# Kernel tuning notes

Hardware: AMD Instinct MI355X
Metric: run time of the kernel (lower is better)

The kernel has to match this reference:

```python
import jax, jax.numpy as jnp
import numpy as np

TF_ALPHA = 0.125  # teacher-forcing blend used in forward()


def setup_inputs() -> dict:
    key = jax.random.key(0)
    ks = jax.random.split(key, 6)
    B, T, dx, dz, dy = 512, 1024, 32, 64, 256
    return {
        "X": jax.random.normal(ks[0], (B, T, dx), dtype=jnp.float32),
        "A": (jax.random.normal(ks[1], (dz,), dtype=jnp.float32) * 0.1),
        "W1": jax.random.normal(ks[2], (dz, dy), dtype=jnp.float32) / np.sqrt(dy).astype(np.float32),
        "W2": jax.random.normal(ks[3], (dy, dz), dtype=jnp.float32) / np.sqrt(dz).astype(np.float32),
        "h1": jax.random.normal(ks[4], (dz,), dtype=jnp.float32) * 0.01,
        "h2": jax.random.normal(ks[5], (dy,), dtype=jnp.float32) * 0.01,
    }


def reference(X, A, W1, W2, h1, h2):
    # X: (batch, time, dim_x); shallow-PLRNN, dim_x_proj=0, no mean centering, no inputs.
    B, T, dx = X.shape
    dz = A.shape[0]

    def teacher_force(z, f, alpha):
        # blend forcing signal into first dx latent dims where f is not NaN
        blend = alpha * f + (1.0 - alpha) * z[:, :dx]
        return z.at[:, :dx].set(jnp.where(jnp.isnan(f), z[:, :dx], blend))

    # z0 = teacher_force(zeros, X[:,0], alpha=1)
    z0 = teacher_force(jnp.zeros((B, dz), X.dtype), X[:, 0], 1.0)

    Xt = jnp.transpose(X, (1, 0, 2))  # (T, B, dx)

    def step(z, x_t):
        zf = teacher_force(z, x_t, TF_ALPHA)
        # shallow-PLRNN: z' = A*z + W1 @ relu(W2 @ z + h2) + h1
        hidden = jax.nn.relu(jnp.einsum('yz,bz->by', W2, zf) + h2)
        z_new = A * zf + jnp.einsum('zy,by->bz', W1, hidden) + h1
        return z_new, z_new

    _, Z = jax.lax.scan(step, z0, Xt)          # (T, B, dz)
    Z = jnp.transpose(Z, (1, 0, 2))            # (B, T, dz)
    return Z[:, :, :dx]                        # output = first dim_x latent dims
```

## Files before the change

kernel.cpp:

```cpp
#include <hip/hip_runtime.h>

#define BB 512
#define TT 1024
#define DX 32
#define DZ 64
#define DY 256
#define ALPHA 0.125f

template<int CTRL>
__device__ __forceinline__ float qperm_add(float x) {
    int p = __builtin_amdgcn_update_dpp(0, __float_as_int(x), CTRL, 0xF, 0xF, true);
    return x + __int_as_float(p);
}
__device__ __forceinline__ float quad_allreduce(float x) {
    x = qperm_add<0xB1>(x);
    x = qperm_add<0x4E>(x);
    return x;
}

__global__ __launch_bounds__(256, 2)
void plrnn_scan(const float* __restrict__ X, const float* __restrict__ A,
                const float* __restrict__ W1, const float* __restrict__ W2,
                const float* __restrict__ h1, const float* __restrict__ h2,
                float* __restrict__ out) {
    const int b   = blockIdx.x;
    const int tid = threadIdx.x;

    const int j  = tid >> 2;
    const int s  = tid & 3;
    const int p  = (tid >> 2) & 15;
    const int c  = tid & 3;
    const int wv = tid >> 6;
    const int s2 = (wv << 2) | c;

    __shared__ float zf_s[DZ];
    __shared__ float hid_s[DY];
    __shared__ float part_s[4 * 68];

    float4 w2c[16];
    float4 w1c[16];
#pragma unroll
    for (int k = 0; k < 16; ++k) {
        w2c[k] = make_float4(W2[(4 * j + 0) * DZ + 16 * s + k],
                             W2[(4 * j + 1) * DZ + 16 * s + k],
                             W2[(4 * j + 2) * DZ + 16 * s + k],
                             W2[(4 * j + 3) * DZ + 16 * s + k]);
        w1c[k] = make_float4(W1[(4 * p + 0) * DY + 16 * s2 + k],
                             W1[(4 * p + 1) * DY + 16 * s2 + k],
                             W1[(4 * p + 2) * DY + 16 * s2 + k],
                             W1[(4 * p + 3) * DY + 16 * s2 + k]);
    }
    const float4 h2q = make_float4(h2[4 * j + 0], h2[4 * j + 1],
                                   h2[4 * j + 2], h2[4 * j + 3]);
    const float Ar  = (tid < DZ) ? A[tid]  : 0.0f;
    const float h1r = (tid < DZ) ? h1[tid] : 0.0f;

    const float* Xb = X   + (size_t)b * TT * DX;
    float*       Ob = out + (size_t)b * TT * DX;

    float zfreg = 0.0f;
    if (tid < DZ) {
        float zf = 0.0f;
        if (tid < DX) { float x0 = Xb[tid]; zf = (x0 == x0) ? x0 : 0.0f; }
        zfreg = zf;
        zf_s[tid] = zf;
    }
    __syncthreads();

    for (int t = 0; t < TT; ++t) {
        float xnext = 0.0f;
        if (tid < DX && (t + 1) < TT) xnext = Xb[(t + 1) * DX + tid];

        float zl[16];
        {
            const float4* zp = (const float4*)zf_s + 4 * s;
            *(float4*)&zl[0]  = zp[0];
            *(float4*)&zl[4]  = zp[1];
            *(float4*)&zl[8]  = zp[2];
            *(float4*)&zl[12] = zp[3];
        }
        float ax = 0.f, ay = 0.f, az = 0.f, aw = 0.f;
#pragma unroll
        for (int k = 0; k < 16; ++k) {
            ax = fmaf(w2c[k].x, zl[k], ax);
            ay = fmaf(w2c[k].y, zl[k], ay);
            az = fmaf(w2c[k].z, zl[k], az);
            aw = fmaf(w2c[k].w, zl[k], aw);
        }
        ax = quad_allreduce(ax);
        ay = quad_allreduce(ay);
        az = quad_allreduce(az);
        aw = quad_allreduce(aw);
        if (s == 0) {
            float4 hv = make_float4(fmaxf(ax + h2q.x, 0.f), fmaxf(ay + h2q.y, 0.f),
                                    fmaxf(az + h2q.z, 0.f), fmaxf(aw + h2q.w, 0.f));
            *(float4*)&hid_s[4 * j] = hv;
        }
        __syncthreads();

        float hl[16];
        {
            const float4* hp = (const float4*)hid_s + 4 * s2;
            *(float4*)&hl[0]  = hp[0];
            *(float4*)&hl[4]  = hp[1];
            *(float4*)&hl[8]  = hp[2];
            *(float4*)&hl[12] = hp[3];
        }
        float px = 0.f, py = 0.f, pz = 0.f, pw = 0.f;
#pragma unroll
        for (int k = 0; k < 16; ++k) {
            px = fmaf(w1c[k].x, hl[k], px);
            py = fmaf(w1c[k].y, hl[k], py);
            pz = fmaf(w1c[k].z, hl[k], pz);
            pw = fmaf(w1c[k].w, hl[k], pw);
        }
        px = quad_allreduce(px);
        py = quad_allreduce(py);
        pz = quad_allreduce(pz);
        pw = quad_allreduce(pw);
        if (c == 0) {
            *(float4*)&part_s[wv * 68 + 4 * p] = make_float4(px, py, pz, pw);
        }
        __syncthreads();

        if (tid < DZ) {
            float ssum = (part_s[tid] + part_s[68 + tid]) +
                         (part_s[136 + tid] + part_s[204 + tid]);
            float znew = fmaf(Ar, zfreg, ssum + h1r);
            float zf = znew;
            if (tid < DX) {
                Ob[t * DX + tid] = znew;
                zf = (xnext == xnext) ? fmaf(ALPHA, xnext, (1.0f - ALPHA) * znew)
                                      : znew;
            }
            zfreg = zf;
            zf_s[tid] = zf;
        }
        __syncthreads();
    }
}

extern "C" void kernel_launch(void* const* d_in, const int* in_sizes, int n_in,
                              void* d_out, int out_size, void* d_ws, size_t ws_size,
                              hipStream_t stream) {
    const float* X  = (const float*)d_in[0];
    const float* A  = (const float*)d_in[1];
    const float* W1 = (const float*)d_in[2];
    const float* W2 = (const float*)d_in[3];
    const float* h1 = (const float*)d_in[4];
    const float* h2 = (const float*)d_in[5];
    float* out = (float*)d_out;

    plrnn_scan<<<BB, 256, 0, stream>>>(X, A, W1, W2, h1, h2, out);
}
```

Before: 888.5 us.

## Repartition PLRNN step across 512 threads and drop the partial-sum barrier

Doubles the block to 512 threads so each thread holds half as many weights and runs a 32-FMA dot product per matvec instead of 64. Each hidden unit is computed by a lane pair, and each latent output by a group of 8 lanes reduced entirely with DPP ops. This removes the shared-memory partial-sum stage and one of the three barriers per time step. The hidden buffer is padded per wave to avoid LDS bank conflicts. In exchange there are more waves per CU and more threads taking part in each barrier.

```diff
diff --git a/kernel.cpp b/kernel.cpp
--- a/kernel.cpp
+++ b/kernel.cpp
@@ -6,19 +6,15 @@
 #define DZ 64
 #define DY 256
 #define ALPHA 0.125f
+#define HP 36
 
 template<int CTRL>
-__device__ __forceinline__ float qperm_add(float x) {
+__device__ __forceinline__ float dpp_add(float x) {
     int p = __builtin_amdgcn_update_dpp(0, __float_as_int(x), CTRL, 0xF, 0xF, true);
     return x + __int_as_float(p);
 }
-__device__ __forceinline__ float quad_allreduce(float x) {
-    x = qperm_add<0xB1>(x);
-    x = qperm_add<0x4E>(x);
-    return x;
-}
 
-__global__ __launch_bounds__(256, 2)
+__global__ __launch_bounds__(512, 4)
 void plrnn_scan(const float* __restrict__ X, const float* __restrict__ A,
                 const float* __restrict__ W1, const float* __restrict__ W2,
                 const float* __restrict__ h1, const float* __restrict__ h2,
@@ -26,115 +22,85 @@
     const int b   = blockIdx.x;
     const int tid = threadIdx.x;
 
-    const int j  = tid >> 2;
-    const int s  = tid & 3;
-    const int p  = (tid >> 2) & 15;
-    const int c  = tid & 3;
-    const int wv = tid >> 6;
-    const int s2 = (wv << 2) | c;
+    const int y    = tid >> 1;
+    const int half = tid & 1;
+    const int z    = tid >> 3;
+    const int oct  = tid & 7;
+    const int wv   = tid >> 6;
 
     __shared__ float zf_s[DZ];
-    __shared__ float hid_s[DY];
-    __shared__ float part_s[4 * 68];
+    __shared__ float hid_s[8 * HP];
 
-    float4 w2c[16];
-    float4 w1c[16];
+    float4 w2r[8];
+    float4 w1r[8];
 #pragma unroll
-    for (int k = 0; k < 16; ++k) {
-        w2c[k] = make_float4(W2[(4 * j + 0) * DZ + 16 * s + k],
-                             W2[(4 * j + 1) * DZ + 16 * s + k],
-                             W2[(4 * j + 2) * DZ + 16 * s + k],
-                             W2[(4 * j + 3) * DZ + 16 * s + k]);
-        w1c[k] = make_float4(W1[(4 * p + 0) * DY + 16 * s2 + k],
-                             W1[(4 * p + 1) * DY + 16 * s2 + k],
-                             W1[(4 * p + 2) * DY + 16 * s2 + k],
-                             W1[(4 * p + 3) * DY + 16 * s2 + k]);
+    for (int j = 0; j < 8; ++j) {
+        w2r[j] = *(const float4*)&W2[y * DZ + 32 * half + 4 * j];
+        w1r[j] = *(const float4*)&W1[z * DY + 32 * oct + 4 * j];
     }
-    const float4 h2q = make_float4(h2[4 * j + 0], h2[4 * j + 1],
-                                   h2[4 * j + 2], h2[4 * j + 3]);
-    const float Ar  = (tid < DZ) ? A[tid]  : 0.0f;
-    const float h1r = (tid < DZ) ? h1[tid] : 0.0f;
+    const float h2r = h2[y];
+    const float Ar  = A[z];
+    const float h1r = h1[z];
 
     const float* Xb = X   + (size_t)b * TT * DX;
     float*       Ob = out + (size_t)b * TT * DX;
 
     float zfreg = 0.0f;
-    if (tid < DZ) {
+    if (oct == 0) {
         float zf = 0.0f;
-        if (tid < DX) { float x0 = Xb[tid]; zf = (x0 == x0) ? x0 : 0.0f; }
+        if (z < DX) { float x0 = Xb[z]; zf = (x0 == x0) ? x0 : 0.0f; }
         zfreg = zf;
-        zf_s[tid] = zf;
+        zf_s[z] = zf;
     }
     __syncthreads();
 
+    const int hidx = wv * HP + (y & 31);
+    const float* w2f = (const float*)w2r;
+    const float* w1f = (const float*)w1r;
+
     for (int t = 0; t < TT; ++t) {
         float xnext = 0.0f;
-        if (tid < DX && (t + 1) < TT) xnext = Xb[(t + 1) * DX + tid];
+        if (oct == 0 && z < DX && (t + 1) < TT) xnext = Xb[(t + 1) * DX + z];
 
-        float zl[16];
-        {
-            const float4* zp = (const float4*)zf_s + 4 * s;
-            *(float4*)&zl[0]  = zp[0];
-            *(float4*)&zl[4]  = zp[1];
-            *(float4*)&zl[8]  = zp[2];
-            *(float4*)&zl[12] = zp[3];
+        const float4* zp = (const float4*)(zf_s + 32 * half);
+        float a0 = 0.f, a1 = 0.f, a2 = 0.f, a3 = 0.f;
+#pragma unroll
+        for (int j = 0; j < 8; ++j) {
+            float4 v = zp[j];
+            a0 = fmaf(w2f[4 * j + 0], v.x, a0);
+            a1 = fmaf(w2f[4 * j + 1], v.y, a1);
+            a2 = fmaf(w2f[4 * j + 2], v.z, a2);
+            a3 = fmaf(w2f[4 * j + 3], v.w, a3);
         }
-        float ax = 0.f, ay = 0.f, az = 0.f, aw = 0.f;
-#pragma unroll
-        for (int k = 0; k < 16; ++k) {
-            ax = fmaf(w2c[k].x, zl[k], ax);
-            ay = fmaf(w2c[k].y, zl[k], ay);
-            az = fmaf(w2c[k].z, zl[k], az);
-            aw = fmaf(w2c[k].w, zl[k], aw);
-        }
-        ax = quad_allreduce(ax);
-        ay = quad_allreduce(ay);
-        az = quad_allreduce(az);
-        aw = quad_allreduce(aw);
-        if (s == 0) {
-            float4 hv = make_float4(fmaxf(ax + h2q.x, 0.f), fmaxf(ay + h2q.y, 0.f),
-                                    fmaxf(az + h2q.z, 0.f), fmaxf(aw + h2q.w, 0.f));
-            *(float4*)&hid_s[4 * j] = hv;
-        }
+        float d1 = (a0 + a1) + (a2 + a3);
+        d1 = dpp_add<0xB1>(d1);
+        if (half == 0) hid_s[hidx] = fmaxf(d1 + h2r, 0.0f);
         __syncthreads();
 
-        float hl[16];
-        {
-            const float4* hp = (const float4*)hid_s + 4 * s2;
-            *(float4*)&hl[0]  = hp[0];
-            *(float4*)&hl[4]  = hp[1];
-            *(float4*)&hl[8]  = hp[2];
-            *(float4*)&hl[12] = hp[3];
+        const float4* hp = (const float4*)(hid_s + HP * oct);
+        float p0 = 0.f, p1 = 0.f, p2 = 0.f, p3 = 0.f;
+#pragma unroll
+        for (int j = 0; j < 8; ++j) {
+            float4 v = hp[j];
+            p0 = fmaf(w1f[4 * j + 0], v.x, p0);
+            p1 = fmaf(w1f[4 * j + 1], v.y, p1);
+            p2 = fmaf(w1f[4 * j + 2], v.z, p2);
+            p3 = fmaf(w1f[4 * j + 3], v.w, p3);
         }
-        float px = 0.f, py = 0.f, pz = 0.f, pw = 0.f;
-#pragma unroll
-        for (int k = 0; k < 16; ++k) {
-            px = fmaf(w1c[k].x, hl[k], px);
-            py = fmaf(w1c[k].y, hl[k], py);
-            pz = fmaf(w1c[k].z, hl[k], pz);
-            pw = fmaf(w1c[k].w, hl[k], pw);
-        }
-        px = quad_allreduce(px);
-        py = quad_allreduce(py);
-        pz = quad_allreduce(pz);
-        pw = quad_allreduce(pw);
-        if (c == 0) {
-            *(float4*)&part_s[wv * 68 + 4 * p] = make_float4(px, py, pz, pw);
-        }
-        __syncthreads();
-
-        if (tid < DZ) {
-            float ssum = (part_s[tid] + part_s[68 + tid]) +
-                         (part_s[136 + tid] + part_s[204 + tid]);
-            float znew = fmaf(Ar, zfreg, ssum + h1r);
+        float d2 = (p0 + p1) + (p2 + p3);
+        d2 = dpp_add<0xB1>(d2);
+        d2 = dpp_add<0x4E>(d2);
+        d2 = dpp_add<0x141>(d2);
+        if (oct == 0) {
+            float znew = fmaf(Ar, zfreg, d2 + h1r);
             float zf = znew;
-            if (tid < DX) {
-                Ob[t * DX + tid] = znew;
+            if (z < DX) {
+                Ob[t * DX + z] = znew;
                 zf = (xnext == xnext) ? fmaf(ALPHA, xnext, (1.0f - ALPHA) * znew)
                                       : znew;
             }
             zfreg = zf;
-            zf_s[tid] = zf;
+            zf_s[z] = zf;
         }
         __syncthreads();
     }
@@ -151,5 +117,5 @@
     const float* h2 = (const float*)d_in[5];
     float* out = (float*)d_out;
 
-    plrnn_scan<<<BB, 256, 0, stream>>>(X, A, W1, W2, h1, h2, out);
+    plrnn_scan<<<BB, 512, 0, stream>>>(X, A, W1, W2, h1, h2, out);
 }
```

Result: faster. 820.7 us (-7.6%).
